# Optimization experiments

Hardware: AMD Instinct MI355X
Metric: run time of the kernel (lower is better)

The kernel has to match this reference:

```python
import jax, jax.numpy as jnp
import numpy as np

B, S, H, DH = 64, 300, 4, 32   # batch, seq, heads, head_dim
D = H * DH                     # hidden = 128
L = 8                          # num_hidden_layers
SPAN = 8                       # max_relative_positions (att_span)
EPS = 1e-7                     # DebertaConfig layer_norm_eps default


def _ln(x, s, b):
    mu = x.mean(-1, keepdims=True)
    var = ((x - mu) ** 2).mean(-1, keepdims=True)
    return (x - mu) * jax.lax.rsqrt(var + EPS) * s + b


def _gelu(x):
    return jax.nn.gelu(x, approximate=False)  # torch nn.GELU / HF 'gelu' (erf)


def setup_inputs():
    ks = iter(jax.random.split(jax.random.key(0), 48))
    w = lambda shape: jax.random.normal(next(ks), shape, jnp.float32) * 0.02
    return dict(
        inputs=jax.random.uniform(next(ks), (B, S, 4), jnp.float32),
        mask=jnp.ones((B, S), jnp.float32),
        emb_W1=w((3, 64)), emb_b1=w((64,)),
        emb_W2=w((64, D)), emb_b2=w((D,)),
        emb_W3=w((D, D)), emb_b3=w((D,)),
        tok_emb=w((2, D)),
        emb_ln_s=jnp.ones((D,), jnp.float32), emb_ln_b=jnp.zeros((D,), jnp.float32),
        rel_emb=w((2 * SPAN, D)),
        qkv_W=w((L, D, 3 * D)), q_bias=w((L, D)), v_bias=w((L, D)),
        pos_k_W=w((L, D, D)), pos_q_W=w((L, D, D)), pos_q_b=w((L, D)),
        attn_out_W=w((L, D, D)), attn_out_b=w((L, D)),
        ln1_s=jnp.ones((L, D), jnp.float32), ln1_b=jnp.zeros((L, D), jnp.float32),
        ffn_W1=w((L, D, 512)), ffn_b1=w((L, 512)),
        ffn_W2=w((L, 512, D)), ffn_b2=w((L, D)),
        ln2_s=jnp.ones((L, D), jnp.float32), ln2_b=jnp.zeros((L, D), jnp.float32),
        rec_W1=w((D, D)), rec_b1=w((D,)),
        rec_W2=w((D, 64)), rec_b2=w((64,)),
        rec_W3=w((64, 5)), rec_b3=w((5,)),
        conn_W=w((S * 5, 2500)), conn_b=w((2500,)),
    )


def reference(inputs, mask, emb_W1, emb_b1, emb_W2, emb_b2, emb_W3, emb_b3,
              tok_emb, emb_ln_s, emb_ln_b, rel_emb,
              qkv_W, q_bias, v_bias, pos_k_W, pos_q_W, pos_q_b,
              attn_out_W, attn_out_b, ln1_s, ln1_b,
              ffn_W1, ffn_b1, ffn_W2, ffn_b2, ln2_s, ln2_b,
              rec_W1, rec_b1, rec_W2, rec_b2, rec_W3, rec_b3,
              conn_W, conn_b):
    # ---- embedding MLP on first 3 feature columns ----
    e = _gelu(inputs[..., :3] @ emb_W1 + emb_b1)
    e = _gelu(e @ emb_W2 + emb_b2)
    e = _gelu(e @ emb_W3 + emb_b3)
    tok = inputs[..., 3].astype(jnp.int32)            # token_type_ids
    e = _ln(e + tok_emb[tok], emb_ln_s, emb_ln_b)     # position_biased_input=False
    x = e * mask[..., None]                           # DebertaEmbeddings mask mult

    # ---- relative position indices (q_size == k_size == S) ----
    rel = jnp.arange(S)[:, None] - jnp.arange(S)[None, :]
    c2p_idx = jnp.clip(rel + SPAN, 0, 2 * SPAN - 1)   # [S,S]
    p2c_idx = jnp.clip(-rel + SPAN, 0, 2 * SPAN - 1)  # [S,S]
    mask4 = (mask[:, None, :, None] * mask[:, None, None, :]) > 0  # [B,1,S,S]
    neg = jnp.finfo(x.dtype).min
    scale = jnp.sqrt(jnp.asarray(DH * 3, x.dtype))    # scale_factor = 1+len([c2p,p2c])

    for l in range(L):
        qkv = (x @ qkv_W[l]).reshape(B, S, H, 3, DH)  # in_proj (no bias)
        q = qkv[..., 0, :].transpose(0, 2, 1, 3) + q_bias[l].reshape(H, DH)[None, :, None, :]
        k = qkv[..., 1, :].transpose(0, 2, 1, 3)
        v = qkv[..., 2, :].transpose(0, 2, 1, 3) + v_bias[l].reshape(H, DH)[None, :, None, :]
        q = q / scale
        scores = jnp.einsum('bhqd,bhkd->bhqk', q, k)  # content-to-content
        # content-to-position
        pos_k = (rel_emb @ pos_k_W[l]).reshape(2 * SPAN, H, DH).transpose(1, 0, 2)  # [H,16,DH]
        c2p = jnp.einsum('bhqd,hrd->bhqr', q, pos_k)  # [B,H,S,16]
        scores = scores + jnp.take_along_axis(c2p, c2p_idx[None, None], axis=-1)
        # position-to-content
        pos_q = ((rel_emb @ pos_q_W[l]) + pos_q_b[l]).reshape(2 * SPAN, H, DH).transpose(1, 0, 2) / scale
        p2c = jnp.einsum('bhkd,hrd->bhkr', k, pos_q)  # [B,H,S,16]
        scores = scores + jnp.swapaxes(jnp.take_along_axis(p2c, p2c_idx[None, None], axis=-1), -1, -2)
        # XSoftmax
        probs = jnp.where(mask4, jax.nn.softmax(jnp.where(mask4, scores, neg), axis=-1), 0.0)
        ctx = jnp.einsum('bhqk,bhkd->bhqd', probs, v).transpose(0, 2, 1, 3).reshape(B, S, D)
        x = _ln(ctx @ attn_out_W[l] + attn_out_b[l] + x, ln1_s[l], ln1_b[l])
        h = _gelu(x @ ffn_W1[l] + ffn_b1[l])
        x = _ln(h @ ffn_W2[l] + ffn_b2[l] + x, ln2_s[l], ln2_b[l])

    # ---- reconstruction MLP + connection ----
    r = _gelu(x @ rec_W1 + rec_b1)
    r = _gelu(r @ rec_W2 + rec_b2)
    r = _gelu(r @ rec_W3 + rec_b3)                    # [B,S,5]
    out = r.reshape(B, S * 5) @ conn_W + conn_b       # [B,2500]
    return out.reshape(-1, 50, 50)
```

## Files before the change

kernel.cpp:

```cpp
#include <hip/hip_runtime.h>
#include <hip/hip_bf16.h>
#include <math.h>

#define Bq 64
#define Sq 300
#define NH 4
#define DHd 32
#define Dd 128
#define NL 8
#define FF 512
#define NIN 36
#define SP 304
#define SPX 320

typedef __attribute__((ext_vector_type(8))) short bf16x8;
typedef __attribute__((ext_vector_type(4))) float f32x4;

__device__ __forceinline__ float gelu_f(float x) {
    return 0.5f * x * (1.0f + erff(x * 0.70710678118654752f));
}
__device__ __forceinline__ bool bf16_mode(const unsigned* maskw) {
    return maskw[0] == 0x3F803F80u;
}

struct ConvArgs {
    const void* src[NIN];
    float* dst[NIN];
    int n[NIN];
};

__global__ void convert_kernel(ConvArgs a, const unsigned* maskw) {
    bool bfm = bf16_mode(maskw);
    int bi = blockIdx.y;
    int n = a.n[bi];
    float* dst = a.dst[bi];
    int stride = gridDim.x * blockDim.x;
    int i0 = blockIdx.x * blockDim.x + threadIdx.x;
    if (bfm) {
        const __hip_bfloat16* s = (const __hip_bfloat16*)a.src[bi];
        for (int i = i0; i < n; i += stride) dst[i] = __bfloat162float(s[i]);
    } else {
        const float* s = (const float*)a.src[bi];
        for (int i = i0; i < n; i += stride) dst[i] = s[i];
    }
}

__global__ void pack_kernel(const float* __restrict__ W1all, const float* __restrict__ W2all,
                            const float* __restrict__ Wqall, const float* __restrict__ Woall,
                            const float* __restrict__ Wr1, const float* __restrict__ Wr2,
                            const float* __restrict__ We2, const float* __restrict__ We3,
                            __hip_bfloat16* __restrict__ P1, __hip_bfloat16* __restrict__ P2,
                            __hip_bfloat16* __restrict__ Pq, __hip_bfloat16* __restrict__ Po,
                            __hip_bfloat16* __restrict__ Pr1, __hip_bfloat16* __restrict__ Pr2,
                            __hip_bfloat16* __restrict__ Pe2, __hip_bfloat16* __restrict__ Pe3) {
    int l = blockIdx.y;
    int which = blockIdx.z;
    if (which >= 4 && l != 0) return;
    int K = (which == 1) ? 512 : ((which == 6) ? 64 : 128);
    int N = (which == 0) ? 512 : (which == 1 ? 128 : (which == 2 ? 384 : (which == 5 ? 64 : 128)));
    int slots = (K / 32) * (N / 16) * 64;
    int idx = blockIdx.x * 256 + threadIdx.x;
    if (idx >= slots) return;
    int lane = idx & 63;
    int nkt = K / 32;
    int kt = (idx >> 6) % nkt;
    int nt = (idx >> 6) / nkt;
    const float* W; __hip_bfloat16* P;
    switch (which) {
        case 0:  W = W1all + (size_t)l * 128 * 512; P = P1 + (size_t)l * 65536; break;
        case 1:  W = W2all + (size_t)l * 512 * 128; P = P2 + (size_t)l * 65536; break;
        case 2:  W = Wqall + (size_t)l * 128 * 384; P = Pq + (size_t)l * 49152; break;
        case 3:  W = Woall + (size_t)l * 128 * 128; P = Po + (size_t)l * 16384; break;
        case 4:  W = Wr1; P = Pr1; break;
        case 5:  W = Wr2; P = Pr2; break;
        case 6:  W = We2; P = Pe2; break;
        default: W = We3; P = Pe3; break;
    }
    P += (size_t)idx * 8;
    int n = nt * 16 + (lane & 15);
    int k0 = kt * 32 + (lane >> 4) * 8;
    #pragma unroll
    for (int j = 0; j < 8; j++) P[j] = __float2bfloat16(W[(size_t)(k0 + j) * N + n]);
}

__global__ __launch_bounds__(256) void embed_mfma_kernel(
        const float* __restrict__ inp, const float* __restrict__ mask,
        const float* __restrict__ W1, const float* __restrict__ b1,
        const __hip_bfloat16* __restrict__ Pe2, const float* __restrict__ b2,
        const __hip_bfloat16* __restrict__ Pe3, const float* __restrict__ b3,
        const float* __restrict__ tok_emb,
        const float* __restrict__ ln_s, const float* __restrict__ ln_b,
        float* __restrict__ x) {
    int blk = blockIdx.x;
    int t = threadIdx.x;
    int w = t >> 6, lane = t & 63;
    int row0 = blk * 16;
    __shared__ float f[16][4];
    __shared__ __align__(16) __hip_bfloat16 e1a[16 * 72];
    __shared__ __align__(16) __hip_bfloat16 e2a[16 * 136];
    __shared__ float dbuf[16 * 132];
    if (t < 64) f[t >> 2][t & 3] = inp[(size_t)(row0 + (t >> 2)) * 4 + (t & 3)];
    __syncthreads();
    {
        int r1 = t >> 4, n0 = (t & 15) * 4;
        float f0 = f[r1][0], f1 = f[r1][1], f2 = f[r1][2];
        #pragma unroll
        for (int j = 0; j < 4; j++) {
            int n = n0 + j;
            float a = b1[n] + f0 * W1[n] + f1 * W1[64 + n] + f2 * W1[128 + n];
            e1a[r1 * 72 + n] = __float2bfloat16(gelu_f(a));
        }
    }
    __syncthreads();
    int m = lane & 15, quad = lane >> 4;
    bf16x8 a2[2];
    #pragma unroll
    for (int kt = 0; kt < 2; kt++) a2[kt] = *(bf16x8*)&e1a[m * 72 + kt * 32 + quad * 8];
    #pragma unroll
    for (int nt0 = 0; nt0 < 2; nt0++) {
        int nt = w * 2 + nt0;
        f32x4 acc = {0.f, 0.f, 0.f, 0.f};
        const bf16x8* bp = (const bf16x8*)(Pe2 + (size_t)nt * 2 * 512);
        #pragma unroll
        for (int kt = 0; kt < 2; kt++) {
            bf16x8 bfr = bp[kt * 64 + lane];
            acc = __builtin_amdgcn_mfma_f32_16x16x32_bf16(a2[kt], bfr, acc, 0, 0, 0);
        }
        int n = nt * 16 + m;
        float bb = b2[n];
        #pragma unroll
        for (int r = 0; r < 4; r++)
            e2a[(quad * 4 + r) * 136 + n] = __float2bfloat16(gelu_f(acc[r] + bb));
    }
    __syncthreads();
    bf16x8 a3[4];
    #pragma unroll
    for (int kt = 0; kt < 4; kt++) a3[kt] = *(bf16x8*)&e2a[m * 136 + kt * 32 + quad * 8];
    f32x4 acc2[2] = {{0.f,0.f,0.f,0.f}, {0.f,0.f,0.f,0.f}};
    #pragma unroll
    for (int kt = 0; kt < 4; kt++) {
        #pragma unroll
        for (int nt0 = 0; nt0 < 2; nt0++) {
            int nt = w * 2 + nt0;
            bf16x8 bfr = ((const bf16x8*)(Pe3 + (size_t)nt * 4 * 512))[kt * 64 + lane];
            acc2[nt0] = __builtin_amdgcn_mfma_f32_16x16x32_bf16(a3[kt], bfr, acc2[nt0], 0, 0, 0);
        }
    }
    #pragma unroll
    for (int nt0 = 0; nt0 < 2; nt0++) {
        int n = (w * 2 + nt0) * 16 + m;
        float bb = b3[n];
        #pragma unroll
        for (int r = 0; r < 4; r++) {
            int row = quad * 4 + r;
            int tok = (int)f[row][3];
            dbuf[row * 132 + n] = gelu_f(acc2[nt0][r] + bb) + tok_emb[tok * 128 + n];
        }
    }
    __syncthreads();
    #pragma unroll
    for (int rr = 0; rr < 4; rr++) {
        int row = w * 4 + rr;
        int c0 = lane, c1 = lane + 64;
        float y0 = dbuf[row * 132 + c0];
        float y1 = dbuf[row * 132 + c1];
        float sm = y0 + y1;
        #pragma unroll
        for (int o = 32; o > 0; o >>= 1) sm += __shfl_xor(sm, o);
        float mu = sm * (1.0f / 128.0f);
        float d0 = y0 - mu, d1 = y1 - mu;
        float vv = d0 * d0 + d1 * d1;
        #pragma unroll
        for (int o = 32; o > 0; o >>= 1) vv += __shfl_xor(vv, o);
        float rstd = rsqrtf(vv * (1.0f / 128.0f) + 1e-7f);
        float mk = mask[row0 + row];
        x[(size_t)(row0 + row) * 128 + c0] = (d0 * rstd * ln_s[c0] + ln_b[c0]) * mk;
        x[(size_t)(row0 + row) * 128 + c1] = (d1 * rstd * ln_s[c1] + ln_b[c1]) * mk;
    }
}

__global__ __launch_bounds__(512) void qkv_mfma_kernel(const float* __restrict__ x,
                                                       const __hip_bfloat16* __restrict__ Pq,
                                                       const float* __restrict__ qb, const float* __restrict__ vb,
                                                       __hip_bfloat16* __restrict__ qbf,
                                                       __hip_bfloat16* __restrict__ kbf,
                                                       __hip_bfloat16* __restrict__ vT) {
    int blk = blockIdx.x;
    int t = threadIdx.x;
    int w = t >> 6, lane = t & 63;
    int row0 = blk * 32;
    __shared__ __align__(16) __hip_bfloat16 xa[32 * 136];
    for (int i = t; i < 1024; i += 512) {
        float4 v4 = ((const float4*)(x + (size_t)row0 * 128))[i];
        int r = i >> 5, c4 = (i & 31) * 4;
        __hip_bfloat16* d = &xa[r * 136 + c4];
        d[0] = __float2bfloat16(v4.x); d[1] = __float2bfloat16(v4.y);
        d[2] = __float2bfloat16(v4.z); d[3] = __float2bfloat16(v4.w);
    }
    __syncthreads();
    int m = lane & 15, quad = lane >> 4;
    bf16x8 a1[2][4];
    #pragma unroll
    for (int mt = 0; mt < 2; mt++)
        #pragma unroll
        for (int kt = 0; kt < 4; kt++)
            a1[mt][kt] = *(bf16x8*)&xa[(mt * 16 + m) * 136 + kt * 32 + quad * 8];
    const float inv_scale = 0.10206207261596576f;
    #pragma unroll
    for (int nt0 = 0; nt0 < 3; nt0++) {
        int nt = w * 3 + nt0;
        f32x4 acc[2] = {{0.f,0.f,0.f,0.f}, {0.f,0.f,0.f,0.f}};
        const bf16x8* bp = (const bf16x8*)(Pq + (size_t)nt * 4 * 512);
        #pragma unroll
        for (int kt = 0; kt < 4; kt++) {
            bf16x8 bfr = bp[kt * 64 + lane];
            #pragma unroll
            for (int mt = 0; mt < 2; mt++)
                acc[mt] = __builtin_amdgcn_mfma_f32_16x16x32_bf16(a1[mt][kt], bfr, acc[mt], 0, 0, 0);
        }
        int n = nt * 16 + m;
        int h = n / 96, mm = (n % 96) / 32, d = n % 32;
        float qbv = qb[h * 32 + d], vbv = vb[h * 32 + d];
        #pragma unroll
        for (int mt = 0; mt < 2; mt++) {
            #pragma unroll
            for (int r = 0; r < 4; r++) {
                int row = row0 + mt * 16 + quad * 4 + r;
                int bb = row / Sq, s = row % Sq;
                int bh = bb * NH + h;
                float a = acc[mt][r];
                if (mm == 0) {
                    qbf[((size_t)bh * SP + s) * 32 + d] = __float2bfloat16((a + qbv) * inv_scale);
                } else if (mm == 1) {
                    kbf[((size_t)bh * SP + s) * 32 + d] = __float2bfloat16(a);
                } else {
                    vT[((size_t)bh * 32 + d) * SP + s] = __float2bfloat16(a + vbv);
                }
            }
        }
    }
}

__global__ void pad_kernel(__hip_bfloat16* qbf, __hip_bfloat16* kbf, __hip_bfloat16* vT) {
    int i = blockIdx.x * 256 + threadIdx.x;
    if (i >= 256 * 4 * 32) return;
    int bh = i >> 7, s = Sq + ((i >> 5) & 3), d = i & 31;
    __hip_bfloat16 z = __float2bfloat16(0.0f);
    qbf[((size_t)bh * SP + s) * 32 + d] = z;
    kbf[((size_t)bh * SP + s) * 32 + d] = z;
    vT[((size_t)bh * 32 + d) * SP + s] = z;
}

__global__ void pos_kernel(const float* __restrict__ rel_emb,
                           const float* __restrict__ pkW_all, const float* __restrict__ pqW_all,
                           const float* __restrict__ pqb_all,
                           __hip_bfloat16* __restrict__ poskb, __hip_bfloat16* __restrict__ posqb) {
    int l = blockIdx.y;
    int bi = blockIdx.x;
    int which = bi >> 4;
    int r = bi & 15;
    int t = threadIdx.x;
    __shared__ float re[128];
    re[t] = rel_emb[r * 128 + t];
    __syncthreads();
    const float* W = (which ? pqW_all : pkW_all) + (size_t)l * 128 * 128;
    float a = 0.0f;
    for (int k = 0; k < 128; k++) a += re[k] * W[k * 128 + t];
    int h = t >> 5, d = t & 31;
    size_t o = ((size_t)(l * NH + h) * 16 + r) * 32 + d;
    if (which) { a = (a + pqb_all[l * 128 + t]) * 0.10206207261596576f; posqb[o] = __float2bfloat16(a); }
    else       { poskb[o] = __float2bfloat16(a); }
}

__global__ __launch_bounds__(256) void attn_mfma_kernel(const __hip_bfloat16* __restrict__ qbf,
                                                        const __hip_bfloat16* __restrict__ kbf,
                                                        const __hip_bfloat16* __restrict__ vT,
                                                        const __hip_bfloat16* __restrict__ poskb,
                                                        const __hip_bfloat16* __restrict__ posqb,
                                                        const float* __restrict__ mask,
                                                        __hip_bfloat16* __restrict__ ctxb) {
    int bh = blockIdx.x;
    int b = bh >> 2, h = bh & 3;
    int t = threadIdx.x;
    int w = t >> 6, lane = t & 63;
    int m = lane & 15, quad = lane >> 4;

    __shared__ float p2cS[SPX * 17];
    __shared__ float c2pS[4][16 * 17];
    __shared__ __align__(16) __hip_bfloat16 pT[4][16 * 40];

    {
        bf16x8 pqf = *(const bf16x8*)&posqb[(h * 16 + m) * 32 + quad * 8];
        #pragma unroll
        for (int it = 0; it < 5; it++) {
            int jb = (w + it * 4) * 16;
            bf16x8 kf2 = *(const bf16x8*)&kbf[((size_t)bh * SP + jb + m) * 32 + quad * 8];
            f32x4 pc = __builtin_amdgcn_mfma_f32_16x16x32_bf16(kf2, pqf, (f32x4){0.f,0.f,0.f,0.f}, 0, 0, 0);
            #pragma unroll
            for (int r = 0; r < 4; r++) {
                int j = jb + quad * 4 + r;
                float mv = (j < Sq) ? mask[b * Sq + j] : 0.0f;
                p2cS[j * 17 + m] = (mv > 0.0f) ? pc[r] : -30000.0f;
            }
        }
    }
    __syncthreads();

    int qt = blockIdx.y * 4 + w;
    if (qt >= 19) return;
    int q0 = qt * 16;

    float* c2pW = c2pS[w];
    __hip_bfloat16* pTW = pT[w];

    bf16x8 aq = *(const bf16x8*)&qbf[((size_t)bh * SP + q0 + m) * 32 + quad * 8];

    {
        bf16x8 pkf = *(const bf16x8*)&poskb[(h * 16 + m) * 32 + quad * 8];
        f32x4 cc = __builtin_amdgcn_mfma_f32_16x16x32_bf16(aq, pkf, (f32x4){0.f,0.f,0.f,0.f}, 0, 0, 0);
        #pragma unroll
        for (int r = 0; r < 4; r++) c2pW[(quad * 4 + r) * 17 + m] = cc[r];
    }

    int qi = q0 + m;
    f32x4 oacc[2] = {{0.f,0.f,0.f,0.f}, {0.f,0.f,0.f,0.f}};
    float lacc = 0.0f;

    for (int jt2 = 0; jt2 < 10; jt2++) {
        int j0 = jt2 * 32;
        #pragma unroll
        for (int half = 0; half < 2; half++) {
            int jh = j0 + half * 16;
            bf16x8 kf = *(const bf16x8*)&kbf[((size_t)bh * SP + jh + m) * 32 + quad * 8];
            f32x4 sc = __builtin_amdgcn_mfma_f32_16x16x32_bf16(kf, aq, (f32x4){0.f,0.f,0.f,0.f}, 0, 0, 0);
            int jb2 = jh + quad * 4;
            int base = qi - jb2 + 8;
            __hip_bfloat16 pb[4];
            #pragma unroll
            for (int r = 0; r < 4; r++) {
                int rr = base - r; rr = rr < 0 ? 0 : (rr > 15 ? 15 : rr);
                float sv = sc[r] + c2pW[m * 17 + rr] + p2cS[(jb2 + r) * 17 + rr];
                float p = __expf(sv);
                lacc += p;
                pb[r] = __float2bfloat16(p);
            }
            *(uint2*)&pTW[m * 40 + half * 16 + quad * 4] = *(uint2*)pb;
        }
        bf16x8 ap = *(bf16x8*)&pTW[m * 40 + quad * 8];
        #pragma unroll
        for (int nt = 0; nt < 2; nt++) {
            bf16x8 vf = *(const bf16x8*)&vT[((size_t)bh * 32 + nt * 16 + m) * SP + j0 + quad * 8];
            oacc[nt] = __builtin_amdgcn_mfma_f32_16x16x32_bf16(ap, vf, oacc[nt], 0, 0, 0);
        }
    }

    lacc += __shfl_xor(lacc, 16);
    lacc += __shfl_xor(lacc, 32);
    #pragma unroll
    for (int r = 0; r < 4; r++) {
        int qrow = quad * 4 + r;
        float lr = __shfl(lacc, qrow);
        int qi2 = q0 + qrow;
        float qm = (qi2 < Sq) ? mask[b * Sq + qi2] : 0.0f;
        float inv = (qm > 0.0f && lr > 0.0f) ? 1.0f / lr : 0.0f;
        if (qi2 < Sq) {
            size_t base2 = ((size_t)(b * Sq + qi2)) * 128 + h * 32;
            ctxb[base2 + m]      = __float2bfloat16(oacc[0][r] * inv);
            ctxb[base2 + 16 + m] = __float2bfloat16(oacc[1][r] * inv);
        }
    }
}

__global__ __launch_bounds__(512) void aoffn_mfma_kernel(
        const __hip_bfloat16* __restrict__ ctxb,
        const __hip_bfloat16* __restrict__ Po, const float* __restrict__ ob,
        const float* __restrict__ ln1s, const float* __restrict__ ln1b,
        const __hip_bfloat16* __restrict__ P1, const float* __restrict__ b1,
        const __hip_bfloat16* __restrict__ P2, const float* __restrict__ b2,
        const float* __restrict__ ln2s, const float* __restrict__ ln2b,
        float* __restrict__ x,
        int do_qkv,
        const __hip_bfloat16* __restrict__ Pqn,
        const float* __restrict__ qbn, const float* __restrict__ vbn,
        __hip_bfloat16* __restrict__ qbf, __hip_bfloat16* __restrict__ kbf,
        __hip_bfloat16* __restrict__ vT) {
    int blk = blockIdx.x;
    int t = threadIdx.x;
    int w = t >> 6, lane = t & 63;
    int row0 = blk * 32;

    __shared__ __align__(16) __hip_bfloat16 ca[32 * 136];
    __shared__ __align__(16) char hbuf[32 * 520 * 2];
    __hip_bfloat16* ha = (__hip_bfloat16*)hbuf;
    float* dbuf = (float*)hbuf;

    {
        uint4 cv = ((const uint4*)(ctxb + (size_t)row0 * 128))[t];
        int r = t >> 4, c8 = (t & 15) * 8;
        *(uint4*)&ca[r * 136 + c8] = cv;
    }
    __syncthreads();

    int m = lane & 15, quad = lane >> 4;

    {
        f32x4 acc[2] = {{0.f,0.f,0.f,0.f}, {0.f,0.f,0.f,0.f}};
        const bf16x8* bp = (const bf16x8*)(Po + (size_t)w * 4 * 512);
        #pragma unroll
        for (int kt = 0; kt < 4; kt++) {
            bf16x8 bfr = bp[kt * 64 + lane];
            #pragma unroll
            for (int mt = 0; mt < 2; mt++) {
                bf16x8 a = *(bf16x8*)&ca[(mt * 16 + m) * 136 + kt * 32 + quad * 8];
                acc[mt] = __builtin_amdgcn_mfma_f32_16x16x32_bf16(a, bfr, acc[mt], 0, 0, 0);
            }
        }
        int n = w * 16 + m;
        #pragma unroll
        for (int mt = 0; mt < 2; mt++)
            #pragma unroll
            for (int r = 0; r < 4; r++)
                dbuf[(mt * 16 + quad * 4 + r) * 132 + n] = acc[mt][r];
    }
    __syncthreads();

    float x1a[4], x1b[4];
    #pragma unroll
    for (int rr = 0; rr < 4; rr++) {
        int row = w * 4 + rr;
        int c0 = lane, c1 = lane + 64;
        size_t g = (size_t)(row0 + row) * 128;
        float y0 = dbuf[row * 132 + c0] + ob[c0] + x[g + c0];
        float y1 = dbuf[row * 132 + c1] + ob[c1] + x[g + c1];
        float sm = y0 + y1;
        #pragma unroll
        for (int o = 32; o > 0; o >>= 1) sm += __shfl_xor(sm, o);
        float mu = sm * (1.0f / 128.0f);
        float d0 = y0 - mu, d1 = y1 - mu;
        float vv = d0 * d0 + d1 * d1;
        #pragma unroll
        for (int o = 32; o > 0; o >>= 1) vv += __shfl_xor(vv, o);
        float rstd = rsqrtf(vv * (1.0f / 128.0f) + 1e-7f);
        float o0 = d0 * rstd * ln1s[c0] + ln1b[c0];
        float o1 = d1 * rstd * ln1s[c1] + ln1b[c1];
        x1a[rr] = o0;
        x1b[rr] = o1;
        ca[row * 136 + c0] = __float2bfloat16(o0);
        ca[row * 136 + c1] = __float2bfloat16(o1);
    }
    __syncthreads();

    {
        bf16x8 a1[2][4];
        #pragma unroll
        for (int mt = 0; mt < 2; mt++)
            #pragma unroll
            for (int kt = 0; kt < 4; kt++)
                a1[mt][kt] = *(bf16x8*)&ca[(mt * 16 + m) * 136 + kt * 32 + quad * 8];
        #pragma unroll
        for (int nt0 = 0; nt0 < 4; nt0++) {
            int nt = w * 4 + nt0;
            f32x4 acc[2] = {{0.f,0.f,0.f,0.f}, {0.f,0.f,0.f,0.f}};
            const bf16x8* bp = (const bf16x8*)(P1 + (size_t)nt * 4 * 512);
            #pragma unroll
            for (int kt = 0; kt < 4; kt++) {
                bf16x8 bfr = bp[kt * 64 + lane];
                #pragma unroll
                for (int mt = 0; mt < 2; mt++)
                    acc[mt] = __builtin_amdgcn_mfma_f32_16x16x32_bf16(a1[mt][kt], bfr, acc[mt], 0, 0, 0);
            }
            int n = nt * 16 + m;
            float bb = b1[n];
            #pragma unroll
            for (int mt = 0; mt < 2; mt++)
                #pragma unroll
                for (int r = 0; r < 4; r++)
                    ha[(mt * 16 + quad * 4 + r) * 520 + n] = __float2bfloat16(gelu_f(acc[mt][r] + bb));
        }
    }
    __syncthreads();

    f32x4 acc2[2] = {{0.f,0.f,0.f,0.f}, {0.f,0.f,0.f,0.f}};
    {
        const bf16x8* bp = (const bf16x8*)(P2 + (size_t)w * 16 * 512);
        #pragma unroll
        for (int kt = 0; kt < 16; kt++) {
            bf16x8 bfr = bp[kt * 64 + lane];
            #pragma unroll
            for (int mt = 0; mt < 2; mt++) {
                bf16x8 a = *(bf16x8*)&ha[(mt * 16 + m) * 520 + kt * 32 + quad * 8];
                acc2[mt] = __builtin_amdgcn_mfma_f32_16x16x32_bf16(a, bfr, acc2[mt], 0, 0, 0);
            }
        }
    }
    __syncthreads();
    {
        int n = w * 16 + m;
        #pragma unroll
        for (int mt = 0; mt < 2; mt++)
            #pragma unroll
            for (int r = 0; r < 4; r++)
                dbuf[(mt * 16 + quad * 4 + r) * 132 + n] = acc2[mt][r];
    }
    __syncthreads();

    #pragma unroll
    for (int rr = 0; rr < 4; rr++) {
        int row = w * 4 + rr;
        int c0 = lane, c1 = lane + 64;
        float y0 = dbuf[row * 132 + c0] + b2[c0] + x1a[rr];
        float y1 = dbuf[row * 132 + c1] + b2[c1] + x1b[rr];
        float sm = y0 + y1;
        #pragma unroll
        for (int o = 32; o > 0; o >>= 1) sm += __shfl_xor(sm, o);
        float mu = sm * (1.0f / 128.0f);
        float d0 = y0 - mu, d1 = y1 - mu;
        float vv = d0 * d0 + d1 * d1;
        #pragma unroll
        for (int o = 32; o > 0; o >>= 1) vv += __shfl_xor(vv, o);
        float rstd = rsqrtf(vv * (1.0f / 128.0f) + 1e-7f);
        float o0 = d0 * rstd * ln2s[c0] + ln2b[c0];
        float o1 = d1 * rstd * ln2s[c1] + ln2b[c1];
        x[(size_t)(row0 + row) * 128 + c0] = o0;
        x[(size_t)(row0 + row) * 128 + c1] = o1;
        ca[row * 136 + c0] = __float2bfloat16(o0);
        ca[row * 136 + c1] = __float2bfloat16(o1);
    }
    if (!do_qkv) return;
    __syncthreads();

    {
        bf16x8 aq[2][4];
        #pragma unroll
        for (int mt = 0; mt < 2; mt++)
            #pragma unroll
            for (int kt = 0; kt < 4; kt++)
                aq[mt][kt] = *(bf16x8*)&ca[(mt * 16 + m) * 136 + kt * 32 + quad * 8];
        const float inv_scale = 0.10206207261596576f;
        #pragma unroll
        for (int nt0 = 0; nt0 < 3; nt0++) {
            int nt = w * 3 + nt0;
            f32x4 acc[2] = {{0.f,0.f,0.f,0.f}, {0.f,0.f,0.f,0.f}};
            const bf16x8* bp = (const bf16x8*)(Pqn + (size_t)nt * 4 * 512);
            #pragma unroll
            for (int kt = 0; kt < 4; kt++) {
                bf16x8 bfr = bp[kt * 64 + lane];
                #pragma unroll
                for (int mt = 0; mt < 2; mt++)
                    acc[mt] = __builtin_amdgcn_mfma_f32_16x16x32_bf16(aq[mt][kt], bfr, acc[mt], 0, 0, 0);
            }
            int n = nt * 16 + m;
            int h = n / 96, mm = (n % 96) / 32, d = n % 32;
            float qbv = qbn[h * 32 + d], vbv = vbn[h * 32 + d];
            #pragma unroll
            for (int mt = 0; mt < 2; mt++) {
                #pragma unroll
                for (int r = 0; r < 4; r++) {
                    int row = row0 + mt * 16 + quad * 4 + r;
                    int bb = row / Sq, s = row % Sq;
                    int bh = bb * NH + h;
                    float a = acc[mt][r];
                    if (mm == 0) {
                        qbf[((size_t)bh * SP + s) * 32 + d] = __float2bfloat16((a + qbv) * inv_scale);
                    } else if (mm == 1) {
                        kbf[((size_t)bh * SP + s) * 32 + d] = __float2bfloat16(a);
                    } else {
                        vT[((size_t)bh * 32 + d) * SP + s] = __float2bfloat16(a + vbv);
                    }
                }
            }
        }
    }
}

__global__ __launch_bounds__(256) void rec_mfma_kernel(const float* __restrict__ x,
                                                       const __hip_bfloat16* __restrict__ Pr1,
                                                       const float* __restrict__ b1,
                                                       const __hip_bfloat16* __restrict__ Pr2,
                                                       const float* __restrict__ b2,
                                                       const float* __restrict__ W3, const float* __restrict__ b3,
                                                       float* __restrict__ r3) {
    int blk = blockIdx.x;
    int t = threadIdx.x;
    int w = t >> 6, lane = t & 63;
    int row0 = blk * 16;
    __shared__ __align__(16) __hip_bfloat16 xa[16 * 136];
    __shared__ __align__(16) __hip_bfloat16 ha[16 * 136];
    __shared__ float r2s[16 * 68];
    for (int i = t; i < 512; i += 256) {
        float4 v4 = ((const float4*)(x + (size_t)row0 * 128))[i];
        int r = i >> 5, c4 = (i & 31) * 4;
        __hip_bfloat16* d = &xa[r * 136 + c4];
        d[0] = __float2bfloat16(v4.x); d[1] = __float2bfloat16(v4.y);
        d[2] = __float2bfloat16(v4.z); d[3] = __float2bfloat16(v4.w);
    }
    __syncthreads();
    int m = lane & 15, quad = lane >> 4;

    bf16x8 a1[4];
    #pragma unroll
    for (int kt = 0; kt < 4; kt++) a1[kt] = *(bf16x8*)&xa[m * 136 + kt * 32 + quad * 8];
    #pragma unroll
    for (int nt0 = 0; nt0 < 2; nt0++) {
        int nt = w * 2 + nt0;
        f32x4 acc = {0.f, 0.f, 0.f, 0.f};
        const bf16x8* bp = (const bf16x8*)(Pr1 + (size_t)nt * 4 * 512);
        #pragma unroll
        for (int kt = 0; kt < 4; kt++) {
            bf16x8 bfr = bp[kt * 64 + lane];
            acc = __builtin_amdgcn_mfma_f32_16x16x32_bf16(a1[kt], bfr, acc, 0, 0, 0);
        }
        int n = nt * 16 + m;
        float bb = b1[n];
        #pragma unroll
        for (int r = 0; r < 4; r++)
            ha[(quad * 4 + r) * 136 + n] = __float2bfloat16(gelu_f(acc[r] + bb));
    }
    __syncthreads();

    {
        f32x4 acc = {0.f, 0.f, 0.f, 0.f};
        const bf16x8* bp = (const bf16x8*)(Pr2 + (size_t)w * 4 * 512);
        #pragma unroll
        for (int kt = 0; kt < 4; kt++) {
            bf16x8 a = *(bf16x8*)&ha[m * 136 + kt * 32 + quad * 8];
            bf16x8 bfr = bp[kt * 64 + lane];
            acc = __builtin_amdgcn_mfma_f32_16x16x32_bf16(a, bfr, acc, 0, 0, 0);
        }
        int n = w * 16 + m;
        float bb = b2[n];
        #pragma unroll
        for (int r = 0; r < 4; r++)
            r2s[(quad * 4 + r) * 68 + n] = gelu_f(acc[r] + bb);
    }
    __syncthreads();

    if (t < 80) {
        int row = t / 5, c = t % 5;
        float a = b3[c];
        for (int k = 0; k < 64; k++) a += r2s[row * 68 + k] * W3[k * 5 + c];
        r3[(size_t)(row0 + row) * 5 + c] = gelu_f(a);
    }
}

__global__ void conn_kernel(const float* __restrict__ r3, const float* __restrict__ W,
                            const float* __restrict__ b, void* out, const unsigned* maskw) {
    bool bfm = bf16_mode(maskw);
    int cb = blockIdx.x;
    int bg = blockIdx.y;
    int t = threadIdx.x;
    int cl = t & 63;
    int kq = t >> 6;
    int col = cb * 64 + cl;
    __shared__ float rs[4 * 1500];
    __shared__ float pacc[4 * 64 * 4];
    {
        const float4* src = (const float4*)(r3 + (size_t)bg * 4 * 1500);
        for (int i = t; i < 1500; i += 256) ((float4*)rs)[i] = src[i];
    }
    __syncthreads();
    float acc[4] = {0.f, 0.f, 0.f, 0.f};
    if (col < 2500) {
        for (int k = kq * 4; k < 1500; k += 16) {
            float w0 = W[(size_t)(k + 0) * 2500 + col];
            float w1 = W[(size_t)(k + 1) * 2500 + col];
            float w2 = W[(size_t)(k + 2) * 2500 + col];
            float w3 = W[(size_t)(k + 3) * 2500 + col];
            #pragma unroll
            for (int bb = 0; bb < 4; bb++) {
                float4 rv = *(const float4*)&rs[bb * 1500 + k];
                acc[bb] += rv.x * w0 + rv.y * w1 + rv.z * w2 + rv.w * w3;
            }
        }
    }
    #pragma unroll
    for (int bb = 0; bb < 4; bb++) pacc[(kq * 64 + cl) * 4 + bb] = acc[bb];
    __syncthreads();
    if (kq == 0 && col < 2500) {
        float bv = b[col];
        #pragma unroll
        for (int bb = 0; bb < 4; bb++) {
            float a = bv + pacc[(0 * 64 + cl) * 4 + bb] + pacc[(1 * 64 + cl) * 4 + bb]
                         + pacc[(2 * 64 + cl) * 4 + bb] + pacc[(3 * 64 + cl) * 4 + bb];
            int ob = bg * 4 + bb;
            if (bfm) ((__hip_bfloat16*)out)[(size_t)ob * 2500 + col] = __float2bfloat16(a);
            else     ((float*)out)[(size_t)ob * 2500 + col] = a;
        }
    }
}

extern "C" void kernel_launch(void* const* d_in, const int* in_sizes, int n_in,
                              void* d_out, int out_size, void* d_ws, size_t ws_size,
                              hipStream_t stream) {
    float* ws = (float*)d_ws;

    float* cv[NIN];
    size_t off = 0;
    for (int i = 0; i < NIN; i++) { cv[i] = ws + off; off += (size_t)in_sizes[i]; }

    const float* inp      = cv[0];
    const float* mask     = cv[1];
    const float* emb_W1   = cv[2];
    const float* emb_b1   = cv[3];
    const float* emb_W2   = cv[4];
    const float* emb_b2   = cv[5];
    const float* emb_W3   = cv[6];
    const float* emb_b3   = cv[7];
    const float* tok_emb  = cv[8];
    const float* emb_ln_s = cv[9];
    const float* emb_ln_b = cv[10];
    const float* rel_emb  = cv[11];
    const float* qkv_W    = cv[12];
    const float* q_bias   = cv[13];
    const float* v_bias   = cv[14];
    const float* pos_k_W  = cv[15];
    const float* pos_q_W  = cv[16];
    const float* pos_q_b  = cv[17];
    const float* attn_out_W = cv[18];
    const float* attn_out_b = cv[19];
    const float* ln1_s    = cv[20];
    const float* ln1_b    = cv[21];
    const float* ffn_W1   = cv[22];
    const float* ffn_b1   = cv[23];
    const float* ffn_W2   = cv[24];
    const float* ffn_b2   = cv[25];
    const float* ln2_s    = cv[26];
    const float* ln2_b    = cv[27];
    const float* rec_W1   = cv[28];
    const float* rec_b1   = cv[29];
    const float* rec_W2   = cv[30];
    const float* rec_b2   = cv[31];
    const float* rec_W3   = cv[32];
    const float* rec_b3   = cv[33];
    const float* conn_W   = cv[34];
    const float* conn_b   = cv[35];

    const int NTOK = Bq * Sq;
    float* x    = ws + off;
    float* q    = x    + (size_t)NTOK * 128;
    float* k    = q    + (size_t)Bq * NH * Sq * 32;
    float* ctx  = k    + (size_t)Bq * NH * Sq * 32;
    float* c2p  = ctx  + (size_t)NTOK * 128;
    float* p2c  = c2p  + (size_t)Bq * NH * Sq * 16;
    float* posk = p2c  + (size_t)Bq * NH * Sq * 16;
    float* posq = posk + (size_t)NL * 16 * 128;
    float* r3b  = posq + (size_t)NL * 16 * 128;
    float* endf = r3b  + (size_t)NTOK * 5;
    __hip_bfloat16* P1 = (__hip_bfloat16*)endf;
    __hip_bfloat16* P2 = P1 + (size_t)NL * 65536;
    __hip_bfloat16* Pq = P2 + (size_t)NL * 65536;
    __hip_bfloat16* Po = Pq + (size_t)NL * 49152;
    __hip_bfloat16* qbf = Po + (size_t)NL * 16384;
    __hip_bfloat16* kbf = qbf + (size_t)256 * SP * 32;
    __hip_bfloat16* vTb = kbf + (size_t)256 * SP * 32;
    __hip_bfloat16* Pr1 = vTb + (size_t)256 * SP * 32;
    __hip_bfloat16* Pr2 = Pr1 + 16384;
    __hip_bfloat16* Pe2 = Pr2 + 8192;
    __hip_bfloat16* Pe3 = Pe2 + 8192;
    __hip_bfloat16* Pkb = Pe3 + 16384;
    __hip_bfloat16* Pqb = Pkb + (size_t)NL * 2048;
    __hip_bfloat16* ctxb = (__hip_bfloat16*)ctx;

    const unsigned* maskw = (const unsigned*)d_in[1];

    ConvArgs ca;
    for (int i = 0; i < NIN; i++) {
        ca.src[i] = d_in[i];
        ca.dst[i] = cv[i];
        ca.n[i] = in_sizes[i];
    }
    convert_kernel<<<dim3(256, NIN), 256, 0, stream>>>(ca, maskw);
    pack_kernel<<<dim3(32, NL, 8), 256, 0, stream>>>(ffn_W1, ffn_W2, qkv_W, attn_out_W,
                                                     rec_W1, rec_W2, emb_W2, emb_W3,
                                                     P1, P2, Pq, Po, Pr1, Pr2, Pe2, Pe3);

    embed_mfma_kernel<<<NTOK / 16, 256, 0, stream>>>(inp, mask, emb_W1, emb_b1,
                                                     Pe2, emb_b2, Pe3, emb_b3,
                                                     tok_emb, emb_ln_s, emb_ln_b, x);

    pos_kernel<<<dim3(32, NL), 128, 0, stream>>>(rel_emb, pos_k_W, pos_q_W, pos_q_b, Pkb, Pqb);
    pad_kernel<<<128, 256, 0, stream>>>(qbf, kbf, vTb);

    qkv_mfma_kernel<<<NTOK / 32, 512, 0, stream>>>(x, Pq, q_bias, v_bias, qbf, kbf, vTb);

    for (int l = 0; l < NL; l++) {
        attn_mfma_kernel<<<dim3(256, 5), 256, 0, stream>>>(qbf, kbf, vTb,
                                                           Pkb + (size_t)l * 2048,
                                                           Pqb + (size_t)l * 2048,
                                                           mask, ctxb);
        int ln = (l + 1 < NL) ? (l + 1) : 0;
        aoffn_mfma_kernel<<<NTOK / 32, 512, 0, stream>>>(ctxb,
                                                         Po + (size_t)l * 16384, attn_out_b + l * 128,
                                                         ln1_s + l * 128, ln1_b + l * 128,
                                                         P1 + (size_t)l * 65536, ffn_b1 + l * 512,
                                                         P2 + (size_t)l * 65536, ffn_b2 + l * 128,
                                                         ln2_s + l * 128, ln2_b + l * 128, x,
                                                         (l + 1 < NL) ? 1 : 0,
                                                         Pq + (size_t)ln * 49152,
                                                         q_bias + ln * 128, v_bias + ln * 128,
                                                         qbf, kbf, vTb);
    }

    rec_mfma_kernel<<<NTOK / 16, 256, 0, stream>>>(x, Pr1, rec_b1, Pr2, rec_b2,
                                                   rec_W3, rec_b3, r3b);
    conn_kernel<<<dim3(40, 16), 256, 0, stream>>>(r3b, conn_W, conn_b, d_out, maskw);
}
```

Baseline: 684.5 us.

## Shuffle attention probabilities in registers and prefetch layer weights before barriers

In the attention kernel, the bf16 probability tile now moves into MFMA A-operand layout through cross-lane shuffles instead of a store and reload through per-wave shared memory. In the fused post-attention/FFN/QKV kernel, weight fragments for the output projection, FFN1, FFN2 and the next layer's QKV are loaded from global memory into registers ahead of the barriers and compute phases that use them. The aim is to hide global load latency behind LDS traffic and layernorm work, and to drop the LDS round trip in attention. The cost is more registers, which could lower occupancy or cause spills.

```diff
diff --git a/kernel.cpp b/kernel.cpp
--- a/kernel.cpp
+++ b/kernel.cpp
@@ -287,7 +287,6 @@
 
     __shared__ float p2cS[SPX * 17];
     __shared__ float c2pS[4][16 * 17];
-    __shared__ __align__(16) __hip_bfloat16 pT[4][16 * 40];
 
     {
         bf16x8 pqf = *(const bf16x8*)&posqb[(h * 16 + m) * 32 + quad * 8];
@@ -311,7 +310,6 @@
     int q0 = qt * 16;
 
     float* c2pW = c2pS[w];
-    __hip_bfloat16* pTW = pT[w];
 
     bf16x8 aq = *(const bf16x8*)&qbf[((size_t)bh * SP + q0 + m) * 32 + quad * 8];
 
@@ -326,8 +324,13 @@
     f32x4 oacc[2] = {{0.f,0.f,0.f,0.f}, {0.f,0.f,0.f,0.f}};
     float lacc = 0.0f;
 
+    int srcA = m + ((quad & 1) << 5);
+    int srcB = srcA + 16;
+    int halfn = quad >> 1;
+
     for (int jt2 = 0; jt2 < 10; jt2++) {
         int j0 = jt2 * 32;
+        unsigned hpk[2][2];
         #pragma unroll
         for (int half = 0; half < 2; half++) {
             int jh = j0 + half * 16;
@@ -335,18 +338,33 @@
             f32x4 sc = __builtin_amdgcn_mfma_f32_16x16x32_bf16(kf, aq, (f32x4){0.f,0.f,0.f,0.f}, 0, 0, 0);
             int jb2 = jh + quad * 4;
             int base = qi - jb2 + 8;
-            __hip_bfloat16 pb[4];
+            union { __hip_bfloat16 bv[2]; unsigned u; } p01, p23;
             #pragma unroll
             for (int r = 0; r < 4; r++) {
                 int rr = base - r; rr = rr < 0 ? 0 : (rr > 15 ? 15 : rr);
                 float sv = sc[r] + c2pW[m * 17 + rr] + p2cS[(jb2 + r) * 17 + rr];
                 float p = __expf(sv);
                 lacc += p;
-                pb[r] = __float2bfloat16(p);
-            }
-            *(uint2*)&pTW[m * 40 + half * 16 + quad * 4] = *(uint2*)pb;
-        }
-        bf16x8 ap = *(bf16x8*)&pTW[m * 40 + quad * 8];
+                if (r < 2) p01.bv[r] = __float2bfloat16(p);
+                else       p23.bv[r - 2] = __float2bfloat16(p);
+            }
+            hpk[half][0] = p01.u;
+            hpk[half][1] = p23.u;
+        }
+        unsigned a00 = (unsigned)__shfl((int)hpk[0][0], srcA);
+        unsigned a01 = (unsigned)__shfl((int)hpk[0][1], srcA);
+        unsigned a10 = (unsigned)__shfl((int)hpk[1][0], srcA);
+        unsigned a11 = (unsigned)__shfl((int)hpk[1][1], srcA);
+        unsigned b00 = (unsigned)__shfl((int)hpk[0][0], srcB);
+        unsigned b01 = (unsigned)__shfl((int)hpk[0][1], srcB);
+        unsigned b10 = (unsigned)__shfl((int)hpk[1][0], srcB);
+        unsigned b11 = (unsigned)__shfl((int)hpk[1][1], srcB);
+        union { unsigned u[4]; bf16x8 v; } apu;
+        apu.u[0] = halfn ? a10 : a00;
+        apu.u[1] = halfn ? a11 : a01;
+        apu.u[2] = halfn ? b10 : b00;
+        apu.u[3] = halfn ? b11 : b01;
+        bf16x8 ap = apu.v;
         #pragma unroll
         for (int nt = 0; nt < 2; nt++) {
             bf16x8 vf = *(const bf16x8*)&vT[((size_t)bh * 32 + nt * 16 + m) * SP + j0 + quad * 8];
@@ -394,6 +412,14 @@
     __hip_bfloat16* ha = (__hip_bfloat16*)hbuf;
     float* dbuf = (float*)hbuf;
 
+    int m = lane & 15, quad = lane >> 4;
+
+    bf16x8 bPo[4];
+    {
+        const bf16x8* bp = (const bf16x8*)(Po + (size_t)w * 4 * 512);
+        #pragma unroll
+        for (int kt = 0; kt < 4; kt++) bPo[kt] = bp[kt * 64 + lane];
+    }
     {
         uint4 cv = ((const uint4*)(ctxb + (size_t)row0 * 128))[t];
         int r = t >> 4, c8 = (t & 15) * 8;
@@ -401,18 +427,14 @@
     }
     __syncthreads();
 
-    int m = lane & 15, quad = lane >> 4;
-
     {
         f32x4 acc[2] = {{0.f,0.f,0.f,0.f}, {0.f,0.f,0.f,0.f}};
-        const bf16x8* bp = (const bf16x8*)(Po + (size_t)w * 4 * 512);
         #pragma unroll
         for (int kt = 0; kt < 4; kt++) {
-            bf16x8 bfr = bp[kt * 64 + lane];
             #pragma unroll
             for (int mt = 0; mt < 2; mt++) {
                 bf16x8 a = *(bf16x8*)&ca[(mt * 16 + m) * 136 + kt * 32 + quad * 8];
-                acc[mt] = __builtin_amdgcn_mfma_f32_16x16x32_bf16(a, bfr, acc[mt], 0, 0, 0);
+                acc[mt] = __builtin_amdgcn_mfma_f32_16x16x32_bf16(a, bPo[kt], acc[mt], 0, 0, 0);
             }
         }
         int n = w * 16 + m;
@@ -421,6 +443,12 @@
             #pragma unroll
             for (int r = 0; r < 4; r++)
                 dbuf[(mt * 16 + quad * 4 + r) * 132 + n] = acc[mt][r];
+    }
+    bf16x8 bF1a[8];
+    #pragma unroll
+    for (int i = 0; i < 8; i++) {
+        int nt0 = i >> 2, kt = i & 3;
+        bF1a[i] = ((const bf16x8*)(P1 + (size_t)(w * 4 + nt0) * 4 * 512))[kt * 64 + lane];
     }
     __syncthreads();
 
@@ -448,8 +476,15 @@
         ca[row * 136 + c0] = __float2bfloat16(o0);
         ca[row * 136 + c1] = __float2bfloat16(o1);
     }
-    __syncthreads();
-
+    bf16x8 bF1b[8];
+    #pragma unroll
+    for (int i = 0; i < 8; i++) {
+        int nt0 = 2 + (i >> 2), kt = i & 3;
+        bF1b[i] = ((const bf16x8*)(P1 + (size_t)(w * 4 + nt0) * 4 * 512))[kt * 64 + lane];
+    }
+    __syncthreads();
+
+    bf16x8 bF2a[8], bF2b[8];
     {
         bf16x8 a1[2][4];
         #pragma unroll
@@ -458,18 +493,16 @@
             for (int kt = 0; kt < 4; kt++)
                 a1[mt][kt] = *(bf16x8*)&ca[(mt * 16 + m) * 136 + kt * 32 + quad * 8];
         #pragma unroll
-        for (int nt0 = 0; nt0 < 4; nt0++) {
-            int nt = w * 4 + nt0;
+        for (int nt0 = 0; nt0 < 2; nt0++) {
             f32x4 acc[2] = {{0.f,0.f,0.f,0.f}, {0.f,0.f,0.f,0.f}};
-            const bf16x8* bp = (const bf16x8*)(P1 + (size_t)nt * 4 * 512);
             #pragma unroll
             for (int kt = 0; kt < 4; kt++) {
-                bf16x8 bfr = bp[kt * 64 + lane];
+                bf16x8 bfr = bF1a[nt0 * 4 + kt];
                 #pragma unroll
                 for (int mt = 0; mt < 2; mt++)
                     acc[mt] = __builtin_amdgcn_mfma_f32_16x16x32_bf16(a1[mt][kt], bfr, acc[mt], 0, 0, 0);
             }
-            int n = nt * 16 + m;
+            int n = (w * 4 + nt0) * 16 + m;
             float bb = b1[n];
             #pragma unroll
             for (int mt = 0; mt < 2; mt++)
@@ -477,20 +510,62 @@
                 for (int r = 0; r < 4; r++)
                     ha[(mt * 16 + quad * 4 + r) * 520 + n] = __float2bfloat16(gelu_f(acc[mt][r] + bb));
         }
+        {
+            const bf16x8* bp = (const bf16x8*)(P2 + (size_t)w * 16 * 512);
+            #pragma unroll
+            for (int kt = 0; kt < 8; kt++) bF2a[kt] = bp[kt * 64 + lane];
+        }
+        #pragma unroll
+        for (int nt0 = 2; nt0 < 4; nt0++) {
+            f32x4 acc[2] = {{0.f,0.f,0.f,0.f}, {0.f,0.f,0.f,0.f}};
+            #pragma unroll
+            for (int kt = 0; kt < 4; kt++) {
+                bf16x8 bfr = bF1b[(nt0 - 2) * 4 + kt];
+                #pragma unroll
+                for (int mt = 0; mt < 2; mt++)
+                    acc[mt] = __builtin_amdgcn_mfma_f32_16x16x32_bf16(a1[mt][kt], bfr, acc[mt], 0, 0, 0);
+            }
+            int n = (w * 4 + nt0) * 16 + m;
+            float bb = b1[n];
+            #pragma unroll
+            for (int mt = 0; mt < 2; mt++)
+                #pragma unroll
+                for (int r = 0; r < 4; r++)
+                    ha[(mt * 16 + quad * 4 + r) * 520 + n] = __float2bfloat16(gelu_f(acc[mt][r] + bb));
+        }
+        {
+            const bf16x8* bp = (const bf16x8*)(P2 + (size_t)w * 16 * 512);
+            #pragma unroll
+            for (int kt = 0; kt < 8; kt++) bF2b[kt] = bp[(kt + 8) * 64 + lane];
+        }
     }
     __syncthreads();
 
     f32x4 acc2[2] = {{0.f,0.f,0.f,0.f}, {0.f,0.f,0.f,0.f}};
     {
-        const bf16x8* bp = (const bf16x8*)(P2 + (size_t)w * 16 * 512);
-        #pragma unroll
-        for (int kt = 0; kt < 16; kt++) {
-            bf16x8 bfr = bp[kt * 64 + lane];
+        #pragma unroll
+        for (int kt = 0; kt < 8; kt++) {
             #pragma unroll
             for (int mt = 0; mt < 2; mt++) {
                 bf16x8 a = *(bf16x8*)&ha[(mt * 16 + m) * 520 + kt * 32 + quad * 8];
-                acc2[mt] = __builtin_amdgcn_mfma_f32_16x16x32_bf16(a, bfr, acc2[mt], 0, 0, 0);
-            }
+                acc2[mt] = __builtin_amdgcn_mfma_f32_16x16x32_bf16(a, bF2a[kt], acc2[mt], 0, 0, 0);
+            }
+        }
+        #pragma unroll
+        for (int kt = 8; kt < 16; kt++) {
+            #pragma unroll
+            for (int mt = 0; mt < 2; mt++) {
+                bf16x8 a = *(bf16x8*)&ha[(mt * 16 + m) * 520 + kt * 32 + quad * 8];
+                acc2[mt] = __builtin_amdgcn_mfma_f32_16x16x32_bf16(a, bF2b[kt - 8], acc2[mt], 0, 0, 0);
+            }
+        }
+    }
+    bf16x8 bQ[12];
+    if (do_qkv) {
+        #pragma unroll
+        for (int i = 0; i < 12; i++) {
+            int nt0 = i >> 2, kt = i & 3;
+            bQ[i] = ((const bf16x8*)(Pqn + (size_t)(w * 3 + nt0) * 4 * 512))[kt * 64 + lane];
         }
     }
     __syncthreads();
@@ -541,10 +616,9 @@
         for (int nt0 = 0; nt0 < 3; nt0++) {
             int nt = w * 3 + nt0;
             f32x4 acc[2] = {{0.f,0.f,0.f,0.f}, {0.f,0.f,0.f,0.f}};
-            const bf16x8* bp = (const bf16x8*)(Pqn + (size_t)nt * 4 * 512);
             #pragma unroll
             for (int kt = 0; kt < 4; kt++) {
-                bf16x8 bfr = bp[kt * 64 + lane];
+                bf16x8 bfr = bQ[nt0 * 4 + kt];
                 #pragma unroll
                 for (int mt = 0; mt < 2; mt++)
                     acc[mt] = __builtin_amdgcn_mfma_f32_16x16x32_bf16(aq[mt][kt], bfr, acc[mt], 0, 0, 0);
```

Result: slower. 737.2 us (+7.7%).
